# Kernel tuning notes

Hardware: AMD Instinct MI355X
Metric: run time of the kernel (lower is better)

## Reference

```python
import jax, jax.numpy as jnp
import numpy as np

B, S, D_IN, D_OUT = 4, 2048, 2048, 8192


def setup_inputs() -> dict:
    key = jax.random.key(0)
    k1, k2 = jax.random.split(key)
    x = jax.random.normal(k1, (B, S, D_IN), dtype=jnp.float32)
    weight = jax.random.normal(k2, (D_OUT, D_IN), dtype=jnp.float32) * 0.02
    alpha = jnp.float32(1.0)
    bias = jnp.zeros((D_OUT,), dtype=jnp.float32)
    return {"x": x, "weight": weight, "alpha": alpha, "bias": bias}


def reference(x, weight, alpha, bias):
    # Ternary quantization: delta = 0.7 * mean(|w|); w_q in {-1,0,1} * alpha
    delta = 0.7 * jnp.mean(jnp.abs(weight))
    w_t = jnp.where(weight > delta, jnp.float32(1.0),
                    jnp.where(weight < -delta, jnp.float32(-1.0), jnp.float32(0.0)))
    w_q = w_t * alpha  # [out, in]
    # F.linear: x @ w_q^T + bias
    return jnp.einsum('bsd,od->bso', x, w_q) + bias
```

## Files before the change

kernel.cpp:

```cpp
#include <hip/hip_runtime.h>
#include <hip/hip_bf16.h>
#include <stdint.h>

typedef __attribute__((ext_vector_type(4))) int i32x4;
typedef __attribute__((ext_vector_type(16))) int i32x16;
typedef signed char s8;

#define M_TOT 8192
#define N_TOT 8192
#define K_TOT 2048
#define W_COUNT (N_TOT * K_TOT)
#define X_COUNT (M_TOT * K_TOT)

__global__ void tl_reduce(const float* __restrict__ w, const float* __restrict__ x,
                          double* __restrict__ wsum, float* __restrict__ xmax) {
    const int b = blockIdx.x;
    if (b < 1024) {
        const int tid = b * 256 + threadIdx.x;
        const float4* w4 = (const float4*)w;
        double s = 0.0;
        for (int i = tid; i < W_COUNT / 4; i += 1024 * 256) {
            float4 v = w4[i];
            s += (double)fabsf(v.x) + (double)fabsf(v.y) + (double)fabsf(v.z) + (double)fabsf(v.w);
        }
        #pragma unroll
        for (int off = 32; off > 0; off >>= 1) s += __shfl_down(s, off);
        __shared__ double red[4];
        if ((threadIdx.x & 63) == 0) red[threadIdx.x >> 6] = s;
        __syncthreads();
        if (threadIdx.x == 0) wsum[b] = (red[0] + red[1]) + (red[2] + red[3]);
    } else {
        const int tid = (b - 1024) * 256 + threadIdx.x;
        const float4* x4 = (const float4*)x;
        float m = 0.0f;
        for (int i = tid; i < X_COUNT / 4; i += 1024 * 256) {
            float4 v = x4[i];
            m = fmaxf(m, fmaxf(fmaxf(fabsf(v.x), fabsf(v.y)), fmaxf(fabsf(v.z), fabsf(v.w))));
        }
        #pragma unroll
        for (int off = 32; off > 0; off >>= 1) m = fmaxf(m, __shfl_down(m, off));
        __shared__ float redm[4];
        if ((threadIdx.x & 63) == 0) redm[threadIdx.x >> 6] = m;
        __syncthreads();
        if (threadIdx.x == 0) xmax[b - 1024] = fmaxf(fmaxf(redm[0], redm[1]), fmaxf(redm[2], redm[3]));
    }
}

__global__ void tl_finalize(const double* __restrict__ wsum, const float* __restrict__ xmax,
                            const float* __restrict__ alpha,
                            double* __restrict__ delta, float* __restrict__ qp) {
    const int t = threadIdx.x;
    double s = (wsum[t] + wsum[t + 256]) + (wsum[t + 512] + wsum[t + 768]);
    float m = fmaxf(fmaxf(xmax[t], xmax[t + 256]), fmaxf(xmax[t + 512], xmax[t + 768]));
    #pragma unroll
    for (int off = 32; off > 0; off >>= 1) {
        s += __shfl_down(s, off);
        m = fmaxf(m, __shfl_down(m, off));
    }
    __shared__ double rs[4];
    __shared__ float rm[4];
    if ((t & 63) == 0) { rs[t >> 6] = s; rm[t >> 6] = m; }
    __syncthreads();
    if (t == 0) {
        *delta = 0.7 * (((rs[0] + rs[1]) + (rs[2] + rs[3])) / (double)W_COUNT);
        float mm = fmaxf(fmaxf(rm[0], rm[1]), fmaxf(rm[2], rm[3]));
        qp[0] = 127.0f / mm;
        qp[1] = alpha[0] * (mm / 127.0f);
    }
}

__global__ void tl_tern_w(const float* __restrict__ w, const double* __restrict__ delta_p,
                          s8* __restrict__ wb) {
    const double d = *delta_p;
    const int i = (blockIdx.x * 256 + threadIdx.x) * 16;
    union { s8 c[16]; i32x4 v; } o;
    #pragma unroll
    for (int j = 0; j < 16; j += 4) {
        float4 v = *(const float4*)(w + i + j);
        float f[4] = {v.x, v.y, v.z, v.w};
        #pragma unroll
        for (int r = 0; r < 4; ++r) {
            double wd = (double)f[r];
            o.c[j + r] = wd > d ? 1 : (wd < -d ? -1 : 0);
        }
    }
    *(i32x4*)(wb + i) = o.v;
}

__global__ void tl_quant_x(const float* __restrict__ x, const float* __restrict__ qp,
                           s8* __restrict__ xb) {
    const float inv = qp[0];
    const int i = (blockIdx.x * 256 + threadIdx.x) * 16;
    union { s8 c[16]; i32x4 v; } o;
    #pragma unroll
    for (int j = 0; j < 16; j += 4) {
        float4 v = *(const float4*)(x + i + j);
        float f[4] = {v.x, v.y, v.z, v.w};
        #pragma unroll
        for (int r = 0; r < 4; ++r) {
            int q = (int)__builtin_rintf(f[r] * inv);
            q = q > 127 ? 127 : (q < -127 ? -127 : q);
            o.c[j + r] = (s8)q;
        }
    }
    *(i32x4*)(xb + i) = o.v;
}


#define SB    __builtin_amdgcn_sched_barrier(0)
#define BARR  __builtin_amdgcn_s_barrier()
#define LGKM6 asm volatile("s_waitcnt lgkmcnt(6)" ::: "memory")
#define LGKM0 asm volatile("s_waitcnt lgkmcnt(0)" ::: "memory")
#define VMW(N) asm volatile("s_waitcnt vmcnt(" #N ")" ::: "memory")
#define PRIO1 __builtin_amdgcn_s_setprio(1)
#define PRIO0 __builtin_amdgcn_s_setprio(0)

#define GLDS(SRC, DOFF) __builtin_amdgcn_global_load_lds(                      \
    (const __attribute__((address_space(1))) void*)(SRC),                      \
    (__attribute__((address_space(3))) void*)(lds + (DOFF)), 16, 0, 0)

#define READ6(AR, BR, S, KK) do {                                              \
    _Pragma("unroll") for (int m_ = 0; m_ < 4; ++m_)                           \
        AR[m_] = *(const i32x4*)(lds + (S) * 16384 + wrOff + m_ * 2048 +       \
                                 (lrd ^ ((KK) * 32)));                         \
    _Pragma("unroll") for (int n_ = 0; n_ < 2; ++n_)                           \
        BR[n_] = *(const i32x4*)(lds + 49152 + (S) * 16384 + wcOff + n_ * 2048 + \
                                 (lrd ^ ((KK) * 32)));                         \
} while (0)

#define MMX(AR, BR) do {                                                       \
    _Pragma("unroll") for (int m_ = 0; m_ < 4; ++m_)                           \
    _Pragma("unroll") for (int n_ = 0; n_ < 2; ++n_)                           \
        acc[m_][n_] = __builtin_amdgcn_mfma_i32_32x32x32_i8(                   \
            AR[m_], BR[n_], acc[m_][n_], 0, 0, 0);                             \
} while (0)

#define STG_A(SS, KOFF) do {                                                   \
    GLDS(aSrc + (KOFF), (SS) * 16384 + L);                                     \
    GLDS(aSrc + (KOFF) + 262144, (SS) * 16384 + 8192 + L);                     \
} while (0)
#define STG_B(SS, KOFF) do {                                                   \
    GLDS(bSrc + (KOFF), 49152 + (SS) * 16384 + L);                             \
    GLDS(bSrc + (KOFF) + 262144, 49152 + (SS) * 16384 + 8192 + L);             \
} while (0)

#define TILE(S, SN, SG, KOFF, DOSTG, LAST) do {                                \
    READ6(aN, bN, S, 1);                                                       \
    LGKM6; SB; PRIO1; MMX(aP, bP); PRIO0; SB;                                  \
    VMW(0); BARR; SB;                                                          \
    if (!(LAST)) READ6(aP, bP, SN, 0);                                         \
    if (DOSTG) { STG_A(SG, KOFF); STG_B(SG, KOFF); }                           \
    if (LAST) { LGKM0; } else { LGKM6; }                                       \
    SB; PRIO1; MMX(aN, bN); PRIO0; SB;                                         \
} while (0)

__global__ __launch_bounds__(512, 2) void tl_gemm_i8(
    const s8* __restrict__ A, const s8* __restrict__ Bm,
    const float* __restrict__ qp, const float* __restrict__ bias,
    float* __restrict__ C) {
    __shared__ __attribute__((aligned(128))) char lds[98304];

    const int t = threadIdx.x;
    const int wid = t >> 6;
    const int l = t & 63;
    const int wr = wid >> 2;
    const int wc = wid & 3;

    const int bid = blockIdx.x;
    const int xc = bid & 7;
    const int j = bid >> 3;
    const int tm = xc * 4 + ((j >> 3) & 3);
    const int tn = (j >> 5) * 8 + (j & 7);
    const int row0 = tm * 256, col0 = tn * 256;

    const int L = t * 16;
    const int off = L ^ (((L >> 7) & 3) << 4);
    const int sr = off >> 6;
    const int kb = off & 63;
    const s8* aSrc = A + (size_t)(row0 + sr) * K_TOT + kb;
    const s8* bSrc = Bm + (size_t)(col0 + sr) * K_TOT + kb;

    const int rl = l & 31, kg = l >> 5;
    const int lrd = rl * 64 + ((kg ^ ((rl >> 1) & 3)) << 4);
    const int wrOff = wr * 8192;
    const int wcOff = wc * 4096;

    i32x16 acc[4][2] = {};
    i32x4 aP[4], bP[2], aN[4], bN[2];

    STG_A(0, 0); STG_B(0, 0);
    STG_A(1, 64); STG_B(1, 64);
    VMW(4); BARR; SB;
    READ6(aP, bP, 0, 0);

    int koff = 128;
    #pragma unroll 1
    for (int i = 0; i < 10; ++i) {
        TILE(0, 1, 2, koff, 1, 0); koff += 64;
        TILE(1, 2, 0, koff, 1, 0); koff += 64;
        TILE(2, 0, 1, koff, 1, 0); koff += 64;
    }
    TILE(0, 1, 0, 0, 0, 0);
    TILE(1, 1, 0, 0, 0, 1);

    const float osc = qp[1];
    #pragma unroll
    for (int m_ = 0; m_ < 4; ++m_) {
        const int crow = row0 + wr * 128 + m_ * 32 + kg * 4;
        #pragma unroll
        for (int n_ = 0; n_ < 2; ++n_) {
            const int ccol = col0 + wc * 64 + n_ * 32 + rl;
            const float bv = bias[ccol];
            #pragma unroll
            for (int r = 0; r < 16; ++r) {
                const int row = crow + (r & 3) + 8 * (r >> 2);
                C[(size_t)row * N_TOT + ccol] = (float)acc[m_][n_][r] * osc + bv;
            }
        }
    }
}

extern "C" void kernel_launch(void* const* d_in, const int* in_sizes, int n_in,
                              void* d_out, int out_size, void* d_ws, size_t ws_size,
                              hipStream_t stream) {
    const float* x     = (const float*)d_in[0];
    const float* wgt   = (const float*)d_in[1];
    const float* alpha = (const float*)d_in[2];
    const float* bias  = (const float*)d_in[3];
    float* out = (float*)d_out;

    char* ws = (char*)d_ws;
    double* wsum = (double*)ws;
    float* xmax  = (float*)(ws + 8192);
    double* delta = (double*)(ws + 12288);
    float* qp     = (float*)(ws + 12304);
    s8* xb = (s8*)(ws + 16384);
    s8* wb = (s8*)(ws + 16384 + (size_t)X_COUNT);

    tl_reduce<<<2048, 256, 0, stream>>>(wgt, x, wsum, xmax);
    tl_finalize<<<1, 256, 0, stream>>>(wsum, xmax, alpha, delta, qp);
    tl_tern_w<<<W_COUNT / (256 * 16), 256, 0, stream>>>(wgt, delta, wb);
    tl_quant_x<<<X_COUNT / (256 * 16), 256, 0, stream>>>(x, qp, xb);
    tl_gemm_i8<<<(M_TOT / 256) * (N_TOT / 256), 512, 0, stream>>>(xb, wb, qp, bias, out);
}
```

Baseline: 215.6 us.

## Switch int8 GEMM from 3-stage LDS ring to double-buffered K pipeline

Replaces the three-stage LDS buffer ring with cross-half register prefetch by a two-stage double buffer. Each K tile now reads both k-halves into registers, issues the next tile's global-to-LDS loads, runs the MFMAs and then waits on vmcnt(0) plus a barrier. LDS per block shrinks from 96KB to 64KB. That simplifies the schedule but shortens how far ahead loads run, so global latency can be exposed at the per-tile barrier.

Measured after the change: 219.9 us. About the same (+2.0%).

```diff
diff --git a/kernel.cpp b/kernel.cpp
--- a/kernel.cpp
+++ b/kernel.cpp
@@ -119,20 +119,29 @@
     (const __attribute__((address_space(1))) void*)(SRC),                      \
     (__attribute__((address_space(3))) void*)(lds + (DOFF)), 16, 0, 0)
 
-#define READ6(AR, BR, S, KK) do {                                              \
-    _Pragma("unroll") for (int m_ = 0; m_ < 4; ++m_)                           \
-        AR[m_] = *(const i32x4*)(lds + (S) * 16384 + wrOff + m_ * 2048 +       \
-                                 (lrd ^ ((KK) * 32)));                         \
-    _Pragma("unroll") for (int n_ = 0; n_ < 2; ++n_)                           \
-        BR[n_] = *(const i32x4*)(lds + 49152 + (S) * 16384 + wcOff + n_ * 2048 + \
-                                 (lrd ^ ((KK) * 32)));                         \
-} while (0)
-
-#define MMX(AR, BR) do {                                                       \
+#define RD12(S) do {                                                           \
+    _Pragma("unroll") for (int m_ = 0; m_ < 4; ++m_)                           \
+        aF0[m_] = *(const i32x4*)(lds + (S) * 16384 + wrOff + m_ * 2048 + lrd);\
+    _Pragma("unroll") for (int n_ = 0; n_ < 2; ++n_)                           \
+        bF0[n_] = *(const i32x4*)(lds + 32768 + (S) * 16384 + wcOff + n_ * 2048 + lrd); \
+    _Pragma("unroll") for (int m_ = 0; m_ < 4; ++m_)                           \
+        aF1[m_] = *(const i32x4*)(lds + (S) * 16384 + wrOff + m_ * 2048 + (lrd ^ 32)); \
+    _Pragma("unroll") for (int n_ = 0; n_ < 2; ++n_)                           \
+        bF1[n_] = *(const i32x4*)(lds + 32768 + (S) * 16384 + wcOff + n_ * 2048 + (lrd ^ 32)); \
+} while (0)
+
+#define MM0() do {                                                             \
     _Pragma("unroll") for (int m_ = 0; m_ < 4; ++m_)                           \
     _Pragma("unroll") for (int n_ = 0; n_ < 2; ++n_)                           \
         acc[m_][n_] = __builtin_amdgcn_mfma_i32_32x32x32_i8(                   \
-            AR[m_], BR[n_], acc[m_][n_], 0, 0, 0);                             \
+            aF0[m_], bF0[n_], acc[m_][n_], 0, 0, 0);                           \
+} while (0)
+
+#define MM1() do {                                                             \
+    _Pragma("unroll") for (int m_ = 0; m_ < 4; ++m_)                           \
+    _Pragma("unroll") for (int n_ = 0; n_ < 2; ++n_)                           \
+        acc[m_][n_] = __builtin_amdgcn_mfma_i32_32x32x32_i8(                   \
+            aF1[m_], bF1[n_], acc[m_][n_], 0, 0, 0);                           \
 } while (0)
 
 #define STG_A(SS, KOFF) do {                                                   \
@@ -140,25 +149,25 @@
     GLDS(aSrc + (KOFF) + 262144, (SS) * 16384 + 8192 + L);                     \
 } while (0)
 #define STG_B(SS, KOFF) do {                                                   \
-    GLDS(bSrc + (KOFF), 49152 + (SS) * 16384 + L);                             \
-    GLDS(bSrc + (KOFF) + 262144, 49152 + (SS) * 16384 + 8192 + L);             \
-} while (0)
-
-#define TILE(S, SN, SG, KOFF, DOSTG, LAST) do {                                \
-    READ6(aN, bN, S, 1);                                                       \
-    LGKM6; SB; PRIO1; MMX(aP, bP); PRIO0; SB;                                  \
-    VMW(0); BARR; SB;                                                          \
-    if (!(LAST)) READ6(aP, bP, SN, 0);                                         \
-    if (DOSTG) { STG_A(SG, KOFF); STG_B(SG, KOFF); }                           \
-    if (LAST) { LGKM0; } else { LGKM6; }                                       \
-    SB; PRIO1; MMX(aN, bN); PRIO0; SB;                                         \
+    GLDS(bSrc + (KOFF), 32768 + (SS) * 16384 + L);                             \
+    GLDS(bSrc + (KOFF) + 262144, 32768 + (SS) * 16384 + 8192 + L);             \
+} while (0)
+
+#define KTILE(S, KOFF, DOSTG, GATE) do {                                       \
+    RD12(S);                                                                   \
+    if (DOSTG) { STG_A((S) ^ 1, KOFF); STG_B((S) ^ 1, KOFF); }                 \
+    SB; LGKM6; SB;                                                             \
+    PRIO1; MM0(); PRIO0; SB;                                                   \
+    LGKM0; SB;                                                                 \
+    PRIO1; MM1(); PRIO0; SB;                                                   \
+    GATE; BARR;                                                                \
 } while (0)
 
 __global__ __launch_bounds__(512, 2) void tl_gemm_i8(
     const s8* __restrict__ A, const s8* __restrict__ Bm,
     const float* __restrict__ qp, const float* __restrict__ bias,
     float* __restrict__ C) {
-    __shared__ __attribute__((aligned(128))) char lds[98304];
+    __shared__ __attribute__((aligned(128))) char lds[65536];
 
     const int t = threadIdx.x;
     const int wid = t >> 6;
@@ -186,22 +195,19 @@
     const int wcOff = wc * 4096;
 
     i32x16 acc[4][2] = {};
-    i32x4 aP[4], bP[2], aN[4], bN[2];
+    i32x4 aF0[4], bF0[2], aF1[4], bF1[2];
 
     STG_A(0, 0); STG_B(0, 0);
-    STG_A(1, 64); STG_B(1, 64);
-    VMW(4); BARR; SB;
-    READ6(aP, bP, 0, 0);
-
-    int koff = 128;
+    VMW(0); BARR;
+
+    int koff = 64;
     #pragma unroll 1
-    for (int i = 0; i < 10; ++i) {
-        TILE(0, 1, 2, koff, 1, 0); koff += 64;
-        TILE(1, 2, 0, koff, 1, 0); koff += 64;
-        TILE(2, 0, 1, koff, 1, 0); koff += 64;
-    }
-    TILE(0, 1, 0, 0, 0, 0);
-    TILE(1, 1, 0, 0, 0, 1);
+    for (int i = 0; i < 15; ++i) {
+        KTILE(0, koff, 1, VMW(0)); koff += 64;
+        KTILE(1, koff, 1, VMW(0)); koff += 64;
+    }
+    KTILE(0, koff, 1, VMW(0));
+    KTILE(1, 0, 0, (void)0);
 
     const float osc = qp[1];
     #pragma unroll
```

## Restructure K-loop pipeline to wait on one in-flight tile and issue prefetch earlier

Applied to the files above, without the earlier changes.

Reorders the per-K-tile schedule of the int8 MFMA GEMM main loop. The global-to-LDS prefetch is now issued right after the first half of the MFMAs instead of after the barrier. The barrier gate waits with vmcnt(4) instead of vmcnt(0), so one stage of global loads stays in flight across the barrier, and the tail tiles are handled with dedicated gates. The aim is to hide global load latency behind compute and avoid draining the memory queue every tile, at the cost of a full lgkmcnt(0) wait before each barrier.

New measurement: 207.0 us. 1.04x faster.

```diff
diff --git a/kernel.cpp b/kernel.cpp
--- a/kernel.cpp
+++ b/kernel.cpp
@@ -119,7 +119,7 @@
     (const __attribute__((address_space(1))) void*)(SRC),                      \
     (__attribute__((address_space(3))) void*)(lds + (DOFF)), 16, 0, 0)
 
-#define READ6(AR, BR, S, KK) do {                                              \
+#define RD6(AR, BR, S, KK) do {                                                \
     _Pragma("unroll") for (int m_ = 0; m_ < 4; ++m_)                           \
         AR[m_] = *(const i32x4*)(lds + (S) * 16384 + wrOff + m_ * 2048 +       \
                                  (lrd ^ ((KK) * 32)));                         \
@@ -128,7 +128,7 @@
                                  (lrd ^ ((KK) * 32)));                         \
 } while (0)
 
-#define MMX(AR, BR) do {                                                       \
+#define MM(AR, BR) do {                                                        \
     _Pragma("unroll") for (int m_ = 0; m_ < 4; ++m_)                           \
     _Pragma("unroll") for (int n_ = 0; n_ < 2; ++n_)                           \
         acc[m_][n_] = __builtin_amdgcn_mfma_i32_32x32x32_i8(                   \
@@ -144,14 +144,16 @@
     GLDS(bSrc + (KOFF) + 262144, 49152 + (SS) * 16384 + 8192 + L);             \
 } while (0)
 
-#define TILE(S, SN, SG, KOFF, DOSTG, LAST) do {                                \
-    READ6(aN, bN, S, 1);                                                       \
-    LGKM6; SB; PRIO1; MMX(aP, bP); PRIO0; SB;                                  \
-    VMW(0); BARR; SB;                                                          \
-    if (!(LAST)) READ6(aP, bP, SN, 0);                                         \
+#define KTILE(S, SN, SG, KOFF, DOSTG, GATE, DONEXT) do {                       \
+    RD6(aO, bO, S, 1);                                                         \
+    SB; LGKM6; SB;                                                             \
+    PRIO1; MM(aE, bE); PRIO0; SB;                                              \
     if (DOSTG) { STG_A(SG, KOFF); STG_B(SG, KOFF); }                           \
-    if (LAST) { LGKM0; } else { LGKM6; }                                       \
-    SB; PRIO1; MMX(aN, bN); PRIO0; SB;                                         \
+    SB; LGKM0; SB;                                                             \
+    GATE; BARR; SB;                                                            \
+    if (DONEXT) RD6(aE, bE, SN, 0);                                            \
+    SB;                                                                        \
+    PRIO1; MM(aO, bO); PRIO0; SB;                                              \
 } while (0)
 
 __global__ __launch_bounds__(512, 2) void tl_gemm_i8(
@@ -186,22 +188,22 @@
     const int wcOff = wc * 4096;
 
     i32x16 acc[4][2] = {};
-    i32x4 aP[4], bP[2], aN[4], bN[2];
+    i32x4 aE[4], bE[2], aO[4], bO[2];
 
     STG_A(0, 0); STG_B(0, 0);
     STG_A(1, 64); STG_B(1, 64);
     VMW(4); BARR; SB;
-    READ6(aP, bP, 0, 0);
+    RD6(aE, bE, 0, 0);
 
     int koff = 128;
     #pragma unroll 1
     for (int i = 0; i < 10; ++i) {
-        TILE(0, 1, 2, koff, 1, 0); koff += 64;
-        TILE(1, 2, 0, koff, 1, 0); koff += 64;
-        TILE(2, 0, 1, koff, 1, 0); koff += 64;
-    }
-    TILE(0, 1, 0, 0, 0, 0);
-    TILE(1, 1, 0, 0, 0, 1);
+        KTILE(0, 1, 2, koff, 1, VMW(4), 1); koff += 64;
+        KTILE(1, 2, 0, koff, 1, VMW(4), 1); koff += 64;
+        KTILE(2, 0, 1, koff, 1, VMW(4), 1); koff += 64;
+    }
+    KTILE(0, 1, 0, 0, 0, VMW(0), 1);
+    KTILE(1, 0, 0, 0, 0, (void)0, 0);
 
     const float osc = qp[1];
     #pragma unroll
```

## Pre-swizzle int8 operands into MFMA fragment layout and load directly to registers

Applied to the files above, without the earlier changes.

The quantization kernels now write X and the ternary weights in a fragment-major layout that matches the MFMA operand order, so each lane's 16 bytes are contiguous per fragment. The GEMM drops LDS staging, barriers and swizzled LDS reads entirely. Each wave instead loads its A/B fragments straight from global memory into registers, double-buffered across k-steps with vmcnt gating. This removes LDS traffic and block-wide synchronisation, but gives up cross-wave reuse of the tiles in LDS, so each wave re-reads global/L2 data that other waves also use.

Result: slower. 251.6 us (+16.7%).

```diff
diff --git a/kernel.cpp b/kernel.cpp
--- a/kernel.cpp
+++ b/kernel.cpp
@@ -70,13 +70,17 @@
 }
 
 __global__ void tl_tern_w(const float* __restrict__ w, const double* __restrict__ delta_p,
-                          s8* __restrict__ wb) {
+                          s8* __restrict__ wbF) {
     const double d = *delta_p;
-    const int i = (blockIdx.x * 256 + threadIdx.x) * 16;
+    const int i = blockIdx.x * 256 + threadIdx.x;
+    const int frag = i >> 6, lane = i & 63;
+    const int n = (frag >> 6) * 32 + (lane & 31);
+    const int k = (frag & 63) * 32 + (lane >> 5) * 16;
+    const float* src = w + (size_t)n * K_TOT + k;
     union { s8 c[16]; i32x4 v; } o;
     #pragma unroll
     for (int j = 0; j < 16; j += 4) {
-        float4 v = *(const float4*)(w + i + j);
+        float4 v = *(const float4*)(src + j);
         float f[4] = {v.x, v.y, v.z, v.w};
         #pragma unroll
         for (int r = 0; r < 4; ++r) {
@@ -84,82 +88,65 @@
             o.c[j + r] = wd > d ? 1 : (wd < -d ? -1 : 0);
         }
     }
-    *(i32x4*)(wb + i) = o.v;
+    *(i32x4*)(wbF + (size_t)i * 16) = o.v;
 }
 
 __global__ void tl_quant_x(const float* __restrict__ x, const float* __restrict__ qp,
-                           s8* __restrict__ xb) {
+                           s8* __restrict__ xbF) {
     const float inv = qp[0];
-    const int i = (blockIdx.x * 256 + threadIdx.x) * 16;
-    union { s8 c[16]; i32x4 v; } o;
+    const int i = blockIdx.x * 256 + threadIdx.x;
+    const int row = i >> 7, c = i & 127;
+    const float* src = x + (size_t)row * K_TOT + c * 16;
+    union { s8 c8[16]; i32x4 v; } o;
     #pragma unroll
     for (int j = 0; j < 16; j += 4) {
-        float4 v = *(const float4*)(x + i + j);
+        float4 v = *(const float4*)(src + j);
         float f[4] = {v.x, v.y, v.z, v.w};
         #pragma unroll
         for (int r = 0; r < 4; ++r) {
             int q = (int)__builtin_rintf(f[r] * inv);
             q = q > 127 ? 127 : (q < -127 ? -127 : q);
-            o.c[j + r] = (s8)q;
-        }
-    }
-    *(i32x4*)(xb + i) = o.v;
+            o.c8[j + r] = (s8)q;
+        }
+    }
+    const size_t dst = ((size_t)(row >> 5) * 64 + (c >> 1)) * 1024 +
+                       ((c & 1) * 32 + (row & 31)) * 16;
+    *(i32x4*)(xbF + dst) = o.v;
 }
 
 
 #define SB    __builtin_amdgcn_sched_barrier(0)
-#define BARR  __builtin_amdgcn_s_barrier()
-#define LGKM6 asm volatile("s_waitcnt lgkmcnt(6)" ::: "memory")
-#define LGKM0 asm volatile("s_waitcnt lgkmcnt(0)" ::: "memory")
 #define VMW(N) asm volatile("s_waitcnt vmcnt(" #N ")" ::: "memory")
 #define PRIO1 __builtin_amdgcn_s_setprio(1)
 #define PRIO0 __builtin_amdgcn_s_setprio(0)
 
-#define GLDS(SRC, DOFF) __builtin_amdgcn_global_load_lds(                      \
-    (const __attribute__((address_space(1))) void*)(SRC),                      \
-    (__attribute__((address_space(3))) void*)(lds + (DOFF)), 16, 0, 0)
-
-#define READ6(AR, BR, S, KK) do {                                              \
+#define ISSUE12(NA, NB_, KOFF) do {                                            \
     _Pragma("unroll") for (int m_ = 0; m_ < 4; ++m_)                           \
-        AR[m_] = *(const i32x4*)(lds + (S) * 16384 + wrOff + m_ * 2048 +       \
-                                 (lrd ^ ((KK) * 32)));                         \
+        _Pragma("unroll") for (int h_ = 0; h_ < 2; ++h_)                       \
+            NA[m_][h_] = *(const i32x4*)(aP[m_] + (KOFF) + h_ * 1024);         \
     _Pragma("unroll") for (int n_ = 0; n_ < 2; ++n_)                           \
-        BR[n_] = *(const i32x4*)(lds + 49152 + (S) * 16384 + wcOff + n_ * 2048 + \
-                                 (lrd ^ ((KK) * 32)));                         \
+        _Pragma("unroll") for (int h_ = 0; h_ < 2; ++h_)                       \
+            NB_[n_][h_] = *(const i32x4*)(bP[n_] + (KOFF) + h_ * 1024);        \
 } while (0)
 
-#define MMX(AR, BR) do {                                                       \
+#define MMH(CA, CB, H) do {                                                    \
     _Pragma("unroll") for (int m_ = 0; m_ < 4; ++m_)                           \
     _Pragma("unroll") for (int n_ = 0; n_ < 2; ++n_)                           \
         acc[m_][n_] = __builtin_amdgcn_mfma_i32_32x32x32_i8(                   \
-            AR[m_], BR[n_], acc[m_][n_], 0, 0, 0);                             \
+            CA[m_][H], CB[n_][H], acc[m_][n_], 0, 0, 0);                       \
 } while (0)
 
-#define STG_A(SS, KOFF) do {                                                   \
-    GLDS(aSrc + (KOFF), (SS) * 16384 + L);                                     \
-    GLDS(aSrc + (KOFF) + 262144, (SS) * 16384 + 8192 + L);                     \
-} while (0)
-#define STG_B(SS, KOFF) do {                                                   \
-    GLDS(bSrc + (KOFF), 49152 + (SS) * 16384 + L);                             \
-    GLDS(bSrc + (KOFF) + 262144, 49152 + (SS) * 16384 + 8192 + L);             \
-} while (0)
-
-#define TILE(S, SN, SG, KOFF, DOSTG, LAST) do {                                \
-    READ6(aN, bN, S, 1);                                                       \
-    LGKM6; SB; PRIO1; MMX(aP, bP); PRIO0; SB;                                  \
-    VMW(0); BARR; SB;                                                          \
-    if (!(LAST)) READ6(aP, bP, SN, 0);                                         \
-    if (DOSTG) { STG_A(SG, KOFF); STG_B(SG, KOFF); }                           \
-    if (LAST) { LGKM0; } else { LGKM6; }                                       \
-    SB; PRIO1; MMX(aN, bN); PRIO0; SB;                                         \
+#define TILE(CA, CB, NA, NB_, KOFF, DOISS, GATE) do {                          \
+    if (DOISS) { ISSUE12(NA, NB_, KOFF); }                                     \
+    SB; GATE; SB;                                                              \
+    PRIO1; MMH(CA, CB, 0); PRIO0; SB;                                          \
+    PRIO1; MMH(CA, CB, 1); PRIO0; SB;                                          \
 } while (0)
 
 __global__ __launch_bounds__(512, 2) void tl_gemm_i8(
     const s8* __restrict__ A, const s8* __restrict__ Bm,
     const float* __restrict__ qp, const float* __restrict__ bias,
     float* __restrict__ C) {
-    __shared__ __attribute__((aligned(128))) char lds[98304];
-
     const int t = threadIdx.x;
     const int wid = t >> 6;
     const int l = t & 63;
@@ -173,35 +160,30 @@
     const int tn = (j >> 5) * 8 + (j & 7);
     const int row0 = tm * 256, col0 = tn * 256;
 
-    const int L = t * 16;
-    const int off = L ^ (((L >> 7) & 3) << 4);
-    const int sr = off >> 6;
-    const int kb = off & 63;
-    const s8* aSrc = A + (size_t)(row0 + sr) * K_TOT + kb;
-    const s8* bSrc = Bm + (size_t)(col0 + sr) * K_TOT + kb;
+    const s8* aP[4];
+    const s8* bP[2];
+    #pragma unroll
+    for (int m_ = 0; m_ < 4; ++m_)
+        aP[m_] = A + (size_t)(tm * 8 + wr * 4 + m_) * 65536 + l * 16;
+    #pragma unroll
+    for (int n_ = 0; n_ < 2; ++n_)
+        bP[n_] = Bm + (size_t)(tn * 8 + wc * 2 + n_) * 65536 + l * 16;
 
     const int rl = l & 31, kg = l >> 5;
-    const int lrd = rl * 64 + ((kg ^ ((rl >> 1) & 3)) << 4);
-    const int wrOff = wr * 8192;
-    const int wcOff = wc * 4096;
 
     i32x16 acc[4][2] = {};
-    i32x4 aP[4], bP[2], aN[4], bN[2];
-
-    STG_A(0, 0); STG_B(0, 0);
-    STG_A(1, 64); STG_B(1, 64);
-    VMW(4); BARR; SB;
-    READ6(aP, bP, 0, 0);
-
-    int koff = 128;
+    i32x4 eA[4][2], eB[2][2], oA[4][2], oB[2][2];
+
+    ISSUE12(eA, eB, 0);
+
+    int koff = 2048;
     #pragma unroll 1
-    for (int i = 0; i < 10; ++i) {
-        TILE(0, 1, 2, koff, 1, 0); koff += 64;
-        TILE(1, 2, 0, koff, 1, 0); koff += 64;
-        TILE(2, 0, 1, koff, 1, 0); koff += 64;
-    }
-    TILE(0, 1, 0, 0, 0, 0);
-    TILE(1, 1, 0, 0, 0, 1);
+    for (int i = 0; i < 15; ++i) {
+        TILE(eA, eB, oA, oB, koff, 1, VMW(12)); koff += 2048;
+        TILE(oA, oB, eA, eB, koff, 1, VMW(12)); koff += 2048;
+    }
+    TILE(eA, eB, oA, oB, koff, 1, VMW(12));
+    TILE(oA, oB, eA, eB, 0, 0, VMW(0));
 
     const float osc = qp[1];
     #pragma unroll
```
